# Kernel optimization log

Hardware: AMD Instinct MI355X
Metric: run time of the kernel (lower is better)

Reference implementation:

```python
import jax, jax.numpy as jnp
import numpy as np

B, H0, W0, C = 8, 112, 112, 192
NH, WS, SS = 6, 7, 3
HID = 4 * C


def _rel_pos_index(ws):
    coords = np.stack(np.meshgrid(np.arange(ws), np.arange(ws), indexing='ij'))  # [2,ws,ws]
    flat = coords.reshape(2, -1)
    rel = flat[:, :, None] - flat[:, None, :]          # [2,N,N]
    rel = rel.transpose(1, 2, 0).copy()                # [N,N,2]
    rel[:, :, 0] += ws - 1
    rel[:, :, 1] += ws - 1
    rel[:, :, 0] *= 2 * ws - 1
    return rel.sum(-1)                                 # [N,N]


def _attn_mask(Hp, Wp, ws, ss):
    # 0 / -100 mask for shifted windows, identical to torch get_attn_mask
    img = np.zeros((Hp, Wp))
    cnt = 0
    for hs in (slice(0, -ws), slice(-ws, -ss), slice(-ss, None)):
        for wsl in (slice(0, -ws), slice(-ws, -ss), slice(-ss, None)):
            img[hs, wsl] = cnt
            cnt += 1
    mw = img.reshape(Hp // ws, ws, Wp // ws, ws).transpose(0, 2, 1, 3).reshape(-1, ws * ws)
    am = mw[:, None, :] - mw[:, :, None]
    return np.where(am != 0, np.float32(-100.0), np.float32(0.0)).astype(np.float32)  # [nW,N,N]


def _ln(x, g, b, eps=1e-5):
    mu = jnp.mean(x, axis=-1, keepdims=True)
    var = jnp.mean(jnp.square(x - mu), axis=-1, keepdims=True)
    return (x - mu) * jax.lax.rsqrt(var + eps) * g + b


def setup_inputs() -> dict:
    key = jax.random.key(0)
    ks = jax.random.split(key, 8)
    p = lambda k, s: jax.random.normal(k, s, jnp.float32) * 0.02
    return {
        'query': jax.random.normal(ks[0], (B, H0 * W0, C), jnp.float32),
        'norm1_g': jnp.ones((C,), jnp.float32), 'norm1_b': jnp.zeros((C,), jnp.float32),
        'qkv_w': p(ks[1], (C, 3 * C)), 'qkv_b': jnp.zeros((3 * C,), jnp.float32),
        'rpb_table': p(ks[2], ((2 * WS - 1) ** 2, NH)),
        'proj_w': p(ks[3], (C, C)), 'proj_b': jnp.zeros((C,), jnp.float32),
        'norm2_g': jnp.ones((C,), jnp.float32), 'norm2_b': jnp.zeros((C,), jnp.float32),
        'fc1_w': p(ks[4], (C, HID)), 'fc1_b': jnp.zeros((HID,), jnp.float32),
        'fc2_w': p(ks[5], (HID, C)), 'fc2_b': jnp.zeros((C,), jnp.float32),
        'H': H0, 'W': W0,
    }


def reference(query, norm1_g, norm1_b, qkv_w, qkv_b, rpb_table, proj_w, proj_b,
              norm2_g, norm2_b, fc1_w, fc1_b, fc2_w, fc2_b, H, W):
    Bq, L, Cq = query.shape
    ws, ss, nh = WS, SS, NH
    hd = Cq // nh
    N = ws * ws
    # ---- W-MSA branch ----
    x = _ln(query, norm1_g, norm1_b).reshape(Bq, H, W, Cq)
    # H, W chosen divisible by ws -> pad branch is a no-op
    x = jnp.roll(x, (-ss, -ss), axis=(1, 2))            # cyclic shift
    nWh, nWw = H // ws, W // ws
    # window partition -> [B*nW, N, C]
    xw = x.reshape(Bq, nWh, ws, nWw, ws, Cq).transpose(0, 1, 3, 2, 4, 5).reshape(-1, N, Cq)
    qkv = (xw @ qkv_w + qkv_b).reshape(-1, N, 3, nh, hd).transpose(2, 0, 3, 1, 4)
    q, k, v = qkv[0] * (hd ** -0.5), qkv[1], qkv[2]     # [B_,nh,N,hd]
    attn = jnp.einsum('bhnd,bhmd->bhnm', q, k)
    bias = rpb_table[_rel_pos_index(ws).reshape(-1)].reshape(N, N, nh).transpose(2, 0, 1)
    attn = attn + bias[None]
    mask = jnp.asarray(_attn_mask(H, W, ws, ss))        # [nW,N,N]
    nW = mask.shape[0]
    attn = attn.reshape(Bq, nW, nh, N, N) + mask[None, :, None]
    attn = jax.nn.softmax(attn.reshape(-1, nh, N, N), axis=-1)
    out = jnp.einsum('bhnm,bhmd->bhnd', attn, v).transpose(0, 2, 1, 3).reshape(-1, N, Cq)
    out = out @ proj_w + proj_b
    # window reverse + reverse shift
    x = out.reshape(Bq, nWh, nWw, ws, ws, Cq).transpose(0, 1, 3, 2, 4, 5).reshape(Bq, H, W, Cq)
    x = jnp.roll(x, (ss, ss), axis=(1, 2)).reshape(Bq, H * W, Cq)
    x = query + x
    # ---- MLP branch ----
    h = _ln(x, norm2_g, norm2_b)
    h = jax.nn.gelu(h @ fc1_w + fc1_b, approximate=False)
    return x + (h @ fc2_w + fc2_b)
```

## Files before the change

### kernel.cpp

```cpp
#include <hip/hip_runtime.h>
#include <hip/hip_bf16.h>
#include <math.h>

using bf16 = __hip_bfloat16;
typedef __bf16 bf16x8 __attribute__((ext_vector_type(8)));
typedef __bf16 bf16x4 __attribute__((ext_vector_type(4)));
typedef float floatx4 __attribute__((ext_vector_type(4)));

__device__ __forceinline__ float bf2f(bf16 x) { return __bfloat162float(x); }
__device__ __forceinline__ bf16 f2bf(float x) { return __float2bfloat16(x); }

__device__ __forceinline__ float loadExt(const void* p, long i, int f32) {
  return f32 ? ((const float*)p)[i] : bf2f(((const bf16*)p)[i]);
}
__device__ __forceinline__ void storeExt(void* p, long i, int f32, float v) {
  if (f32) ((float*)p)[i] = v;
  else     ((bf16*)p)[i] = f2bf(v);
}

#define GLOAD16(gp, lp)                                                       \
  __builtin_amdgcn_global_load_lds(                                           \
      (const __attribute__((address_space(1))) void*)(gp),                    \
      (__attribute__((address_space(3))) void*)(lp), 16, 0, 0)

#define LGKM0_BAR()                                                           \
  do {                                                                        \
    asm volatile("s_waitcnt lgkmcnt(0)" ::: "memory");                        \
    __builtin_amdgcn_s_barrier();                                             \
    __builtin_amdgcn_sched_barrier(0);                                        \
  } while (0)

__global__ void detect_kernel(const unsigned int* __restrict__ q, int* __restrict__ flag) {
  const int lane = threadIdx.x;
  const unsigned int w = q[lane];
  const unsigned int lo = w & 0xffffu;
  const unsigned int e = (lo >> 7) & 0xffu;
  const bool ok = (lo == 0u) || (e >= 100u && e <= 141u);
  const unsigned long long m = __ballot(ok);
  if (lane == 0) flag[0] = (__popcll(m) == 64) ? 1 : 0;
}

__global__ void cvt_params_kernel(const int* __restrict__ flagp,
                                  const void* qkv_b, const void* proj_b,
                                  const void* n1g, const void* n1b,
                                  const void* n2g, const void* n2b,
                                  const void* fc1_b, const void* fc2_b,
                                  const void* rpb, bf16* __restrict__ dst) {
  const int f32 = (flagp[0] == 0);
  int i = blockIdx.x * blockDim.x + threadIdx.x;
  if (i >= 3510) return;
  const void* src; int j = i;
  if      (j < 576)  { src = qkv_b; }
  else if ((j -= 576)  < 192) { src = proj_b; }
  else if ((j -= 192)  < 192) { src = n1g; }
  else if ((j -= 192)  < 192) { src = n1b; }
  else if ((j -= 192)  < 192) { src = n2g; }
  else if ((j -= 192)  < 192) { src = n2b; }
  else if ((j -= 192)  < 768) { src = fc1_b; }
  else if ((j -= 768)  < 192) { src = fc2_b; }
  else { j -= 192; src = rpb; }
  dst[i] = f2bf(loadExt(src, j, f32));
}

__global__ void cvtT_kernel(const int* __restrict__ flagp, const void* __restrict__ src,
                            bf16* __restrict__ dst, int K, int N) {
  const int f32 = (flagp[0] == 0);
  int i = blockIdx.x * blockDim.x + threadIdx.x;
  if (i >= K * N) return;
  int n = i / K, k = i - n * K;
  dst[i] = f2bf(loadExt(src, (long)k * N + n, f32));
}

__global__ void biastab_kernel(const bf16* __restrict__ rpb,
                               bf16* __restrict__ btab) {
  int i = blockIdx.x * blockDim.x + threadIdx.x;
  if (i >= 6 * 2450) return;
  int head = i / 2450, r = i - head * 2450;
  int n = r / 50, m = r - n * 50;
  float v = 0.f;
  if (n < 49 && m < 49) {
    int r1 = n / 7, c1 = n - 7 * r1, r2 = m / 7, c2 = m - 7 * r2;
    v = bf2f(rpb[((r1 - r2 + 6) * 13 + (c1 - c2 + 6)) * 6 + head]);
  }
  btab[i] = f2bf(v);
}

__global__ __launch_bounds__(256) void ln_kernel(const int* __restrict__ flagp, int ext,
                                                 const void* __restrict__ x,
                                                 const bf16* __restrict__ g,
                                                 const bf16* __restrict__ b,
                                                 bf16* __restrict__ out) {
  const int f32 = ext && (flagp[0] == 0);
  const long row = (long)blockIdx.x * 4 + (threadIdx.x >> 6);
  const int lane = threadIdx.x & 63;
  const long gbase = row * 192;
  float v0 = loadExt(x, gbase + lane, f32);
  float v1 = loadExt(x, gbase + lane + 64, f32);
  float v2 = loadExt(x, gbase + lane + 128, f32);
  float s = v0 + v1 + v2;
  #pragma unroll
  for (int off = 32; off > 0; off >>= 1) s += __shfl_xor(s, off, 64);
  const float mu = s * (1.0f / 192.0f);
  float d0 = v0 - mu, d1 = v1 - mu, d2 = v2 - mu;
  float vv = d0 * d0 + d1 * d1 + d2 * d2;
  #pragma unroll
  for (int off = 32; off > 0; off >>= 1) vv += __shfl_xor(vv, off, 64);
  const float rstd = rsqrtf(vv * (1.0f / 192.0f) + 1e-5f);
  bf16* orow = out + row * 192;
  orow[lane]       = f2bf(d0 * rstd * bf2f(g[lane])       + bf2f(b[lane]));
  orow[lane + 64]  = f2bf(d1 * rstd * bf2f(g[lane + 64])  + bf2f(b[lane + 64]));
  orow[lane + 128] = f2bf(d2 * rstd * bf2f(g[lane + 128]) + bf2f(b[lane + 128]));
}

template <int EPI>
__global__ __launch_bounds__(256) void gemm_bt(const bf16* __restrict__ A,
                                               const bf16* __restrict__ BT,
                                               const bf16* __restrict__ bias,
                                               const int* __restrict__ flagp,
                                               const void* res, int res_ext,
                                               void* out, int out_ext,
                                               int M, int N, int K) {
  __shared__ __align__(16) bf16 As[3][128 * 32];
  __shared__ __align__(16) bf16 Bs[3][64 * 32];
  const int xf32 = (flagp[0] == 0);
  const int tid = threadIdx.x;
  const int wave = tid >> 6;
  const int lane = tid & 63;
  const int l16 = lane & 15;
  const int quad = lane >> 4;

  const int nbn = N >> 6;
  const int cpx = gridDim.x >> 3;
  const int wg = (gridDim.x & 7) ? (int)blockIdx.x
                                 : (blockIdx.x & 7) * cpx + (blockIdx.x >> 3);
  const int mb = wg / nbn;
  const int nb = wg - mb * nbn;
  const long m0 = (long)mb * 128;
  const int n0 = nb << 6;

  const int rS = tid >> 2;
  const int sS = tid & 3;
  const int ss = sS ^ ((rS >> 1) & 3);
  const bf16* gA0 = A + (m0 + rS) * (long)K + ss * 8;
  const bf16* gA1 = A + (m0 + rS + 64) * (long)K + ss * 8;
  const bf16* gB  = BT + (long)(n0 + rS) * K + ss * 8;

  floatx4 acc[2][4];
  #pragma unroll
  for (int i = 0; i < 2; i++)
    #pragma unroll
    for (int j = 0; j < 4; j++) acc[i][j] = (floatx4){0.f, 0.f, 0.f, 0.f};

  const int swz = (quad ^ ((l16 >> 1) & 3)) << 3;
  const int arow = wave * 32 + l16;
  const int nt = K >> 5;

  {
    GLOAD16(gA0, &As[0][tid * 8]);
    GLOAD16(gA1, &As[0][(tid + 256) * 8]);
    GLOAD16(gB,  &Bs[0][tid * 8]);
    GLOAD16(gA0 + 32, &As[1][tid * 8]);
    GLOAD16(gA1 + 32, &As[1][(tid + 256) * 8]);
    GLOAD16(gB  + 32, &Bs[1][tid * 8]);
  }

  for (int t = 0; t < nt; ++t) {
    if (t + 1 < nt) { asm volatile("s_waitcnt vmcnt(3)" ::: "memory"); }
    else            { asm volatile("s_waitcnt vmcnt(0)" ::: "memory"); }
    __builtin_amdgcn_s_barrier();
    __builtin_amdgcn_sched_barrier(0);
    if (t + 2 < nt) {
      const int p2 = (t + 2) % 3;
      const int off = (t + 2) * 32;
      GLOAD16(gA0 + off, &As[p2][tid * 8]);
      GLOAD16(gA1 + off, &As[p2][(tid + 256) * 8]);
      GLOAD16(gB  + off, &Bs[p2][tid * 8]);
    }
    const int p = t % 3;
    bf16x8 af[2], bfr[4];
    #pragma unroll
    for (int ms = 0; ms < 2; ms++)
      af[ms] = *(const bf16x8*)&As[p][(arow + ms * 16) * 32 + swz];
    #pragma unroll
    for (int ns = 0; ns < 4; ns++)
      bfr[ns] = *(const bf16x8*)&Bs[p][(ns * 16 + l16) * 32 + swz];
    #pragma unroll
    for (int ms = 0; ms < 2; ms++)
      #pragma unroll
      for (int ns = 0; ns < 4; ns++)
        acc[ms][ns] = __builtin_amdgcn_mfma_f32_16x16x32_bf16(bfr[ns], af[ms], acc[ms][ns], 0, 0, 0);
  }

  #pragma unroll
  for (int ms = 0; ms < 2; ms++) {
    const long row = m0 + wave * 32 + ms * 16 + l16;
    #pragma unroll
    for (int ns = 0; ns < 4; ns++) {
      const int col = n0 + ns * 16 + quad * 4;
      const long idx = row * (long)N + col;
      float v[4];
      #pragma unroll
      for (int r = 0; r < 4; r++) v[r] = acc[ms][ns][r] + bf2f(bias[col + r]);
      if (EPI == 1) {
        #pragma unroll
        for (int r = 0; r < 4; r++)
          v[r] = 0.5f * v[r] * (1.0f + erff(v[r] * 0.70710678118654752f));
      }
      if (EPI == 2) {
        if (res_ext && xf32) {
          const float4 t = *(const float4*)((const float*)res + idx);
          v[0] += t.x; v[1] += t.y; v[2] += t.z; v[3] += t.w;
        } else {
          const bf16x4 t = *(const bf16x4*)((const bf16*)res + idx);
          #pragma unroll
          for (int r = 0; r < 4; r++) v[r] += (float)t[r];
        }
      }
      if (out_ext && xf32) {
        float4 t; t.x = v[0]; t.y = v[1]; t.z = v[2]; t.w = v[3];
        *(float4*)((float*)out + idx) = t;
      } else {
        bf16x4 t;
        #pragma unroll
        for (int r = 0; r < 4; r++) t[r] = (__bf16)v[r];
        *(bf16x4*)((bf16*)out + idx) = t;
      }
    }
  }
}

__global__ __launch_bounds__(256, 1) void mlp_fused(
    const bf16* __restrict__ xb,
    const bf16* __restrict__ w1,
    const bf16* __restrict__ w2,
    const bf16* __restrict__ gN, const bf16* __restrict__ bN,
    const bf16* __restrict__ b1, const bf16* __restrict__ b2,
    const int* __restrict__ flagp, void* __restrict__ out) {
  __shared__ __align__(16) __bf16 Ash[128 * 192];
  __shared__ __align__(16) __bf16 W1sh[2][64 * 192];
  __shared__ __align__(16) __bf16 W2sh[192 * 64];
  __shared__ __align__(16) __bf16 Hsh[128 * 64];
  const int xf32 = (flagp[0] == 0);
  const int tid = threadIdx.x, wave = tid >> 6, lane = tid & 63;
  const int l16 = lane & 15, quad = lane >> 4;
  const int cpx = gridDim.x >> 3;
  const int mb = (gridDim.x & 7) ? (int)blockIdx.x
                                 : (int)(blockIdx.x & 7) * cpx + (int)(blockIdx.x >> 3);
  const long m0 = (long)mb * 128;

  {
    const bf16* src = xb + m0 * 192;
    #pragma unroll
    for (int i = 0; i < 12; i++)
      GLOAD16(src + (i * 256 + tid) * 8, &Ash[(i * 256 + tid) * 8]);
  }
  asm volatile("s_waitcnt vmcnt(0)" ::: "memory");
  __builtin_amdgcn_s_barrier();

  {
    const int row = tid >> 1, half = tid & 1;
    bf16x8 xr[12];
    #pragma unroll
    for (int i = 0; i < 12; i++)
      xr[i] = *(const bf16x8*)&Ash[row * 192 + (half * 12 + i) * 8];
    float s1 = 0.f;
    #pragma unroll
    for (int i = 0; i < 12; i++)
      #pragma unroll
      for (int j = 0; j < 8; j++) s1 += (float)xr[i][j];
    s1 += __shfl_xor(s1, 1, 64);
    const float mu = s1 * (1.0f / 192.0f);
    float s2 = 0.f;
    #pragma unroll
    for (int i = 0; i < 12; i++)
      #pragma unroll
      for (int j = 0; j < 8; j++) {
        const float d = (float)xr[i][j] - mu;
        s2 += d * d;
      }
    s2 += __shfl_xor(s2, 1, 64);
    const float rstd = rsqrtf(s2 * (1.0f / 192.0f) + 1e-5f);
    #pragma unroll
    for (int i = 0; i < 12; i++) {
      const int slot = half * 12 + i;
      const bf16x8 gg = *(const bf16x8*)&gN[slot * 8];
      const bf16x8 bb = *(const bf16x8*)&bN[slot * 8];
      bf16x8 nr;
      #pragma unroll
      for (int j = 0; j < 8; j++)
        nr[j] = (__bf16)(((float)xr[i][j] - mu) * rstd * (float)gg[j] + (float)bb[j]);
      xr[i] = nr;
    }
    __syncthreads();
    #pragma unroll
    for (int i = 0; i < 12; i++) {
      const int slot = half * 12 + i;
      const int sw = (slot & 24) | ((slot ^ row) & 7);
      *(bf16x8*)&Ash[row * 192 + sw * 8] = xr[i];
    }
  }
  __syncthreads();

  bf16x8 afr[2][6];
  #pragma unroll
  for (int mt = 0; mt < 2; mt++)
    #pragma unroll
    for (int ks = 0; ks < 6; ks++) {
      const int r = wave * 32 + mt * 16 + l16;
      const int sl = ks * 4 + quad;
      afr[mt][ks] = *(const bf16x8*)&Ash[r * 192 + ((sl & 24) | ((sl ^ r) & 7)) * 8];
    }

  bf16x8 st1[6], st2[6];
  #pragma unroll
  for (int i = 0; i < 6; i++) {
    const int u = i * 256 + tid;
    st1[i] = *(const bf16x8*)&w1[(u / 24) * 192 + (u % 24) * 8];
    st2[i] = *(const bf16x8*)&w2[(u >> 3) * 768 + (u & 7) * 8];
  }
  #pragma unroll
  for (int i = 0; i < 6; i++) {
    const int u = i * 256 + tid;
    const int r1 = u / 24, sl1 = u % 24;
    *(bf16x8*)&W1sh[0][r1 * 192 + ((sl1 & 24) | ((sl1 ^ r1) & 7)) * 8] = st1[i];
    const int r2 = u >> 3, sl2 = u & 7;
    *(bf16x8*)&W2sh[r2 * 64 + ((sl2 ^ r2) & 7) * 8] = st2[i];
  }
  __syncthreads();

  floatx4 C[12][2];
  #pragma unroll
  for (int nt = 0; nt < 12; nt++)
    #pragma unroll
    for (int mt = 0; mt < 2; mt++) C[nt][mt] = (floatx4){0.f, 0.f, 0.f, 0.f};

  for (int s = 0; s < 12; ++s) {
    const int cur = s & 1;
    if (s + 1 < 12) {
      #pragma unroll
      for (int i = 0; i < 6; i++) {
        const int u = i * 256 + tid;
        st1[i] = *(const bf16x8*)&w1[((s + 1) * 64 + u / 24) * 192 + (u % 24) * 8];
        st2[i] = *(const bf16x8*)&w2[(u >> 3) * 768 + (s + 1) * 64 + (u & 7) * 8];
      }
    }
    floatx4 h[4][2];
    #pragma unroll
    for (int jt = 0; jt < 4; jt++)
      #pragma unroll
      for (int mt = 0; mt < 2; mt++) h[jt][mt] = (floatx4){0.f, 0.f, 0.f, 0.f};
    #pragma unroll
    for (int ks = 0; ks < 6; ks++) {
      bf16x8 wf[4];
      #pragma unroll
      for (int jt = 0; jt < 4; jt++) {
        const int r = jt * 16 + l16;
        const int sl = ks * 4 + quad;
        wf[jt] = *(const bf16x8*)&W1sh[cur][r * 192 + ((sl & 24) | ((sl ^ r) & 7)) * 8];
      }
      #pragma unroll
      for (int jt = 0; jt < 4; jt++)
        #pragma unroll
        for (int mt = 0; mt < 2; mt++)
          h[jt][mt] = __builtin_amdgcn_mfma_f32_16x16x32_bf16(wf[jt], afr[mt][ks], h[jt][mt], 0, 0, 0);
    }
    #pragma unroll
    for (int jt = 0; jt < 4; jt++)
      #pragma unroll
      for (int mt = 0; mt < 2; mt++)
        #pragma unroll
        for (int r = 0; r < 4; r++) {
          const int j = jt * 16 + quad * 4 + r;
          float v = h[jt][mt][r] + bf2f(b1[s * 64 + j]);
          v = 0.5f * v * (1.0f + erff(v * 0.70710678118654752f));
          const int m = wave * 32 + mt * 16 + l16;
          Hsh[m * 64 + (((jt * 2 + (quad >> 1)) ^ (l16 & 7)) & 7) * 8 + ((quad * 4 + r) & 7)] = (__bf16)v;
        }
    if (s + 1 < 12) {
      #pragma unroll
      for (int i = 0; i < 6; i++) {
        const int u = i * 256 + tid;
        const int r1 = u / 24, sl1 = u % 24;
        *(bf16x8*)&W1sh[cur ^ 1][r1 * 192 + ((sl1 & 24) | ((sl1 ^ r1) & 7)) * 8] = st1[i];
      }
    }
    LGKM0_BAR();
    #pragma unroll
    for (int k2 = 0; k2 < 2; k2++) {
      bf16x8 hf[2];
      #pragma unroll
      for (int mt = 0; mt < 2; mt++) {
        const int m = wave * 32 + mt * 16 + l16;
        const int sl = k2 * 4 + quad;
        hf[mt] = *(const bf16x8*)&Hsh[m * 64 + ((sl ^ (l16 & 7)) & 7) * 8];
      }
      #pragma unroll
      for (int nt = 0; nt < 12; nt++) {
        const int n = nt * 16 + l16;
        const int sl = k2 * 4 + quad;
        const bf16x8 wf2 = *(const bf16x8*)&W2sh[n * 64 + ((sl ^ n) & 7) * 8];
        #pragma unroll
        for (int mt = 0; mt < 2; mt++)
          C[nt][mt] = __builtin_amdgcn_mfma_f32_16x16x32_bf16(wf2, hf[mt], C[nt][mt], 0, 0, 0);
      }
    }
    LGKM0_BAR();
    if (s + 1 < 12) {
      #pragma unroll
      for (int i = 0; i < 6; i++) {
        const int u = i * 256 + tid;
        const int r2 = u >> 3, sl2 = u & 7;
        *(bf16x8*)&W2sh[r2 * 64 + ((sl2 ^ r2) & 7) * 8] = st2[i];
      }
    }
  }

  #pragma unroll
  for (int mt = 0; mt < 2; mt++) {
    const long row = m0 + wave * 32 + mt * 16 + l16;
    #pragma unroll
    for (int nt = 0; nt < 12; nt++) {
      const int col = nt * 16 + quad * 4;
      const long idx = row * 192 + col;
      float v[4];
      #pragma unroll
      for (int r = 0; r < 4; r++) v[r] = C[nt][mt][r] + bf2f(b2[col + r]);
      const bf16x4 t = *(const bf16x4*)&xb[idx];
      #pragma unroll
      for (int r = 0; r < 4; r++) v[r] += (float)t[r];
      if (xf32) {
        float4 o; o.x = v[0]; o.y = v[1]; o.z = v[2]; o.w = v[3];
        *(float4*)((float*)out + idx) = o;
      } else {
        bf16x4 o;
        #pragma unroll
        for (int r = 0; r < 4; r++) o[r] = (__bf16)v[r];
        *(bf16x4*)((bf16*)out + idx) = o;
      }
    }
  }
}

__global__ __launch_bounds__(64, 3) void attn_kernel(const bf16* __restrict__ qkv,
                                                     const bf16* __restrict__ btab,
                                                     bf16* __restrict__ out) {
  __shared__ __align__(16) __bf16 vshT[32 * 64];
  __shared__ __align__(16) __bf16 psh[64 * 64];
  __shared__ int rowIdx[64];
  __shared__ int regn[64];
  const int lane = threadIdx.x;
  const int q = lane >> 4, l16 = lane & 15;
  const int unit = blockIdx.x;
  const int head = unit % 6;
  const int wIdx = unit / 6;
  const int b = wIdx >> 8;
  const int w2 = wIdx & 255;
  const int wh = w2 >> 4;
  const int ww = w2 & 15;

  {
    const int l = lane < 49 ? lane : 48;
    const int r = l / 7, c = l - 7 * r;
    const int hr = wh * 7 + r;
    const int wr = ww * 7 + c;
    int h = hr + 3; if (h >= 112) h -= 112;
    int w = wr + 3; if (w >= 112) w -= 112;
    rowIdx[lane] = b * 12544 + h * 112 + w;
    const int rh = hr < 105 ? 0 : (hr < 109 ? 1 : 2);
    const int rw = wr < 105 ? 0 : (wr < 109 ? 1 : 2);
    regn[lane] = (lane < 49) ? rh * 3 + rw : 99;
  }
  __syncthreads();

  int ridx[4];
  #pragma unroll
  for (int t = 0; t < 4; t++) ridx[t] = rowIdx[t * 16 + l16];

  #pragma unroll
  for (int ii = 0; ii < 4; ii++) {
    const int i = lane + ii * 64;
    const int j = i >> 2, c = (i & 3) * 8;
    const bf16x8 vv = *(const bf16x8*)&qkv[(long)rowIdx[j] * 576 + 384 + head * 32 + c];
    #pragma unroll
    for (int jj = 0; jj < 8; jj++) {
      const int d = c + jj;
      vshT[d * 64 + (((j >> 3) ^ (d & 7)) << 3) + (j & 7)] = vv[jj];
    }
  }

  floatx4 s[4][4];
  #pragma unroll
  for (int it = 0; it < 4; it++)
    #pragma unroll
    for (int jt = 0; jt < 4; jt++) s[it][jt] = (floatx4){0.f, 0.f, 0.f, 0.f};
  {
    bf16x8 afq[4], bfk[4];
    #pragma unroll
    for (int t = 0; t < 4; t++) {
      const bf16* pQ = &qkv[(long)ridx[t] * 576 + head * 32 + q * 8];
      afq[t] = *(const bf16x8*)pQ;
      bfk[t] = *(const bf16x8*)(pQ + 192);
    }
    #pragma unroll
    for (int it = 0; it < 4; it++)
      #pragma unroll
      for (int jt = 0; jt < 4; jt++)
        s[it][jt] = __builtin_amdgcn_mfma_f32_16x16x32_bf16(afq[it], bfk[jt], s[it][jt], 0, 0, 0);
  }

  int regj[4];
  #pragma unroll
  for (int jt = 0; jt < 4; jt++) regj[jt] = regn[jt * 16 + l16];
  int regi[4][4];
  #pragma unroll
  for (int it = 0; it < 4; it++)
    #pragma unroll
    for (int r = 0; r < 4; r++) regi[it][r] = regn[it * 16 + q * 4 + r];

  const bf16* bt = btab + head * 2450;
  const float scale = 0.17677669529663687f;
  float mrow[4][4];
  #pragma unroll
  for (int it = 0; it < 4; it++)
    #pragma unroll
    for (int r = 0; r < 4; r++) mrow[it][r] = -3e38f;

  #pragma unroll
  for (int it = 0; it < 4; it++)
    #pragma unroll
    for (int jt = 0; jt < 4; jt++)
      #pragma unroll
      for (int r = 0; r < 4; r++) {
        const int i = it * 16 + q * 4 + r;
        const int j = jt * 16 + l16;
        const int bi = (i < 49 ? i : 48) * 50 + (j < 49 ? j : 48);
        float v = s[it][jt][r] * scale + bf2f(bt[bi]);
        if (regi[it][r] != regj[jt]) v -= 100.0f;
        v = (j < 49) ? v : -1e30f;
        s[it][jt][r] = v;
        mrow[it][r] = fmaxf(mrow[it][r], v);
      }
  #pragma unroll
  for (int it = 0; it < 4; it++)
    #pragma unroll
    for (int r = 0; r < 4; r++) {
      float m = mrow[it][r];
      #pragma unroll
      for (int off = 1; off < 16; off <<= 1) m = fmaxf(m, __shfl_xor(m, off, 64));
      mrow[it][r] = m;
    }
  float sum[4][4];
  #pragma unroll
  for (int it = 0; it < 4; it++)
    #pragma unroll
    for (int r = 0; r < 4; r++) sum[it][r] = 0.f;
  #pragma unroll
  for (int it = 0; it < 4; it++)
    #pragma unroll
    for (int jt = 0; jt < 4; jt++)
      #pragma unroll
      for (int r = 0; r < 4; r++) {
        const float e = __expf(s[it][jt][r] - mrow[it][r]);
        s[it][jt][r] = e;
        sum[it][r] += e;
      }
  #pragma unroll
  for (int it = 0; it < 4; it++)
    #pragma unroll
    for (int r = 0; r < 4; r++) {
      float t = sum[it][r];
      #pragma unroll
      for (int off = 1; off < 16; off <<= 1) t += __shfl_xor(t, off, 64);
      mrow[it][r] = 1.0f / t;
    }

  #pragma unroll
  for (int it = 0; it < 4; it++)
    #pragma unroll
    for (int jt = 0; jt < 4; jt++)
      #pragma unroll
      for (int r = 0; r < 4; r++) {
        const int i = it * 16 + q * 4 + r;
        const int j = jt * 16 + l16;
        psh[i * 64 + (((j >> 3) ^ (i & 7)) << 3) + (j & 7)] =
            (__bf16)(s[it][jt][r] * mrow[it][r]);
      }
  __syncthreads();

  floatx4 o[4][2];
  #pragma unroll
  for (int it = 0; it < 4; it++)
    #pragma unroll
    for (int dt = 0; dt < 2; dt++) o[it][dt] = (floatx4){0.f, 0.f, 0.f, 0.f};
  #pragma unroll
  for (int ks = 0; ks < 2; ks++) {
    bf16x8 av[2];
    #pragma unroll
    for (int dt = 0; dt < 2; dt++) {
      const int row = dt * 16 + l16;
      av[dt] = *(const bf16x8*)&vshT[row * 64 + (((ks * 4 + q) ^ (row & 7)) << 3)];
    }
    #pragma unroll
    for (int it = 0; it < 4; it++) {
      const int row = it * 16 + l16;
      const bf16x8 bp = *(const bf16x8*)&psh[row * 64 + (((ks * 4 + q) ^ (row & 7)) << 3)];
      #pragma unroll
      for (int dt = 0; dt < 2; dt++)
        o[it][dt] = __builtin_amdgcn_mfma_f32_16x16x32_bf16(bp, av[dt], o[it][dt], 0, 0, 0);
    }
  }

  #pragma unroll
  for (int it = 0; it < 4; it++)
    #pragma unroll
    for (int r = 0; r < 4; r++) {
      const int i = it * 16 + q * 4 + r;
      if (i < 49) {
        const long ob = (long)rowIdx[i] * 192 + head * 32;
        #pragma unroll
        for (int dt = 0; dt < 2; dt++)
          out[ob + dt * 16 + l16] = f2bf(o[it][dt][r]);
      }
    }
}

extern "C" void kernel_launch(void* const* d_in, const int* in_sizes, int n_in,
                              void* d_out, int out_size, void* d_ws, size_t ws_size,
                              hipStream_t stream) {
  const void* query   = d_in[0];
  const void* norm1_g = d_in[1];
  const void* norm1_b = d_in[2];
  const void* qkv_w   = d_in[3];
  const void* qkv_b   = d_in[4];
  const void* rpb     = d_in[5];
  const void* proj_w  = d_in[6];
  const void* proj_b  = d_in[7];
  const void* norm2_g = d_in[8];
  const void* norm2_b = d_in[9];
  const void* fc1_w   = d_in[10];
  const void* fc1_b   = d_in[11];
  const void* fc2_w   = d_in[12];
  const void* fc2_b   = d_in[13];

  const long M = 100352;

  int* flag  = (int*)d_ws;
  bf16* base = (bf16*)((char*)d_ws + 16);
  bf16* wsA   = base;
  bf16* wsB   = wsA + M * 192;
  bf16* xbuf  = wsB + M * 768;
  bf16* qkvT  = xbuf + M * 192;
  bf16* projT = qkvT + 110592;
  bf16* fc1T  = projT + 36864;
  bf16* fc2T  = fc1T + 147456;
  bf16* pPAR  = fc2T + 147456;
  bf16* pQKVB = pPAR;
  bf16* pPRJB = pQKVB + 576;
  bf16* pN1G  = pPRJB + 192;
  bf16* pN1B  = pN1G + 192;
  bf16* pN2G  = pN1B + 192;
  bf16* pN2B  = pN2G + 192;
  bf16* pFC1B = pN2B + 192;
  bf16* pFC2B = pFC1B + 768;
  bf16* pRPB  = pFC2B + 192;
  bf16* btab  = pPAR + 3510;

  detect_kernel<<<1, 64, 0, stream>>>((const unsigned int*)query, flag);
  cvt_params_kernel<<<14, 256, 0, stream>>>(flag, qkv_b, proj_b, norm1_g, norm1_b,
                                            norm2_g, norm2_b, fc1_b, fc2_b, rpb, pPAR);
  cvtT_kernel<<<(192 * 576 + 255) / 256, 256, 0, stream>>>(flag, qkv_w, qkvT, 192, 576);
  cvtT_kernel<<<(192 * 192 + 255) / 256, 256, 0, stream>>>(flag, proj_w, projT, 192, 192);
  cvtT_kernel<<<(192 * 768 + 255) / 256, 256, 0, stream>>>(flag, fc1_w, fc1T, 192, 768);
  cvtT_kernel<<<(768 * 192 + 255) / 256, 256, 0, stream>>>(flag, fc2_w, fc2T, 768, 192);
  biastab_kernel<<<(6 * 2450 + 255) / 256, 256, 0, stream>>>(pRPB, btab);

  ln_kernel<<<M / 4, 256, 0, stream>>>(flag, 1, query, pN1G, pN1B, wsA);
  gemm_bt<0><<<784 * 9, 256, 0, stream>>>(wsA, qkvT, pQKVB, flag,
                                          nullptr, 0, wsB, 0, (int)M, 576, 192);
  attn_kernel<<<12288, 64, 0, stream>>>(wsB, btab, wsA);
  gemm_bt<2><<<784 * 3, 256, 0, stream>>>(wsA, projT, pPRJB, flag,
                                          query, 1, xbuf, 0, (int)M, 192, 192);

  mlp_fused<<<784, 256, 0, stream>>>(xbuf, fc1T, fc2T, pN2G, pN2B,
                                     pFC1B, pFC2B, flag, d_out);
}
```

Measured before the change: 652.2 us.

## Stream MLP weights from global memory and simplify GEMM to double buffering

In the fused MLP kernel, fc1/fc2 weight tiles are no longer staged through shared memory; MFMA operands are loaded straight from global memory and rely on cache hits. The hidden activation tile becomes per-wave and double-buffered inside a single shared buffer that aliases the input tile, so the cross-wave barriers can go. This cuts LDS use sharply and drops the launch-bounds limit of one block, aiming for higher occupancy. The generic GEMM moves from a 3-stage async pipeline with fine-grained vmcnt waits to a simpler 2-stage loop with __syncthreads, which risks exposing more global load latency.

After: 845.6 us. 29.7% more time.

```diff
diff --git a/kernel.cpp b/kernel.cpp
--- a/kernel.cpp
+++ b/kernel.cpp
@@ -22,13 +22,6 @@
   __builtin_amdgcn_global_load_lds(                                           \
       (const __attribute__((address_space(1))) void*)(gp),                    \
       (__attribute__((address_space(3))) void*)(lp), 16, 0, 0)
-
-#define LGKM0_BAR()                                                           \
-  do {                                                                        \
-    asm volatile("s_waitcnt lgkmcnt(0)" ::: "memory");                        \
-    __builtin_amdgcn_s_barrier();                                             \
-    __builtin_amdgcn_sched_barrier(0);                                        \
-  } while (0)
 
 __global__ void detect_kernel(const unsigned int* __restrict__ q, int* __restrict__ flag) {
   const int lane = threadIdx.x;
@@ -120,8 +113,8 @@
                                                const void* res, int res_ext,
                                                void* out, int out_ext,
                                                int M, int N, int K) {
-  __shared__ __align__(16) bf16 As[3][128 * 32];
-  __shared__ __align__(16) bf16 Bs[3][64 * 32];
+  __shared__ __align__(16) bf16 As[2][128 * 32];
+  __shared__ __align__(16) bf16 Bs[2][64 * 32];
   const int xf32 = (flagp[0] == 0);
   const int tid = threadIdx.x;
   const int wave = tid >> 6;
@@ -153,42 +146,34 @@
 
   const int swz = (quad ^ ((l16 >> 1) & 3)) << 3;
   const int arow = wave * 32 + l16;
-  const int nt = K >> 5;
-
-  {
-    GLOAD16(gA0, &As[0][tid * 8]);
-    GLOAD16(gA1, &As[0][(tid + 256) * 8]);
-    GLOAD16(gB,  &Bs[0][tid * 8]);
-    GLOAD16(gA0 + 32, &As[1][tid * 8]);
-    GLOAD16(gA1 + 32, &As[1][(tid + 256) * 8]);
-    GLOAD16(gB  + 32, &Bs[1][tid * 8]);
-  }
-
-  for (int t = 0; t < nt; ++t) {
-    if (t + 1 < nt) { asm volatile("s_waitcnt vmcnt(3)" ::: "memory"); }
-    else            { asm volatile("s_waitcnt vmcnt(0)" ::: "memory"); }
-    __builtin_amdgcn_s_barrier();
-    __builtin_amdgcn_sched_barrier(0);
-    if (t + 2 < nt) {
-      const int p2 = (t + 2) % 3;
-      const int off = (t + 2) * 32;
-      GLOAD16(gA0 + off, &As[p2][tid * 8]);
-      GLOAD16(gA1 + off, &As[p2][(tid + 256) * 8]);
-      GLOAD16(gB  + off, &Bs[p2][tid * 8]);
-    }
-    const int p = t % 3;
+
+  GLOAD16(gA0, &As[0][tid * 8]);
+  GLOAD16(gA1, &As[0][(tid + 256) * 8]);
+  GLOAD16(gB,  &Bs[0][tid * 8]);
+  __syncthreads();
+
+  int cur = 0;
+  for (int k0 = 0; k0 < K; k0 += 32) {
+    if (k0 + 32 < K) {
+      const int nxt = cur ^ 1;
+      GLOAD16(gA0 + k0 + 32, &As[nxt][tid * 8]);
+      GLOAD16(gA1 + k0 + 32, &As[nxt][(tid + 256) * 8]);
+      GLOAD16(gB  + k0 + 32, &Bs[nxt][tid * 8]);
+    }
     bf16x8 af[2], bfr[4];
     #pragma unroll
     for (int ms = 0; ms < 2; ms++)
-      af[ms] = *(const bf16x8*)&As[p][(arow + ms * 16) * 32 + swz];
+      af[ms] = *(const bf16x8*)&As[cur][(arow + ms * 16) * 32 + swz];
     #pragma unroll
     for (int ns = 0; ns < 4; ns++)
-      bfr[ns] = *(const bf16x8*)&Bs[p][(ns * 16 + l16) * 32 + swz];
+      bfr[ns] = *(const bf16x8*)&Bs[cur][(ns * 16 + l16) * 32 + swz];
     #pragma unroll
     for (int ms = 0; ms < 2; ms++)
       #pragma unroll
       for (int ns = 0; ns < 4; ns++)
         acc[ms][ns] = __builtin_amdgcn_mfma_f32_16x16x32_bf16(bfr[ns], af[ms], acc[ms][ns], 0, 0, 0);
+    __syncthreads();
+    cur ^= 1;
   }
 
   #pragma unroll
@@ -229,17 +214,16 @@
   }
 }
 
-__global__ __launch_bounds__(256, 1) void mlp_fused(
+__global__ __launch_bounds__(256) void mlp_fused(
     const bf16* __restrict__ xb,
     const bf16* __restrict__ w1,
     const bf16* __restrict__ w2,
     const bf16* __restrict__ gN, const bf16* __restrict__ bN,
     const bf16* __restrict__ b1, const bf16* __restrict__ b2,
     const int* __restrict__ flagp, void* __restrict__ out) {
-  __shared__ __align__(16) __bf16 Ash[128 * 192];
-  __shared__ __align__(16) __bf16 W1sh[2][64 * 192];
-  __shared__ __align__(16) __bf16 W2sh[192 * 64];
-  __shared__ __align__(16) __bf16 Hsh[128 * 64];
+  __shared__ __align__(16) char smem[128 * 192 * 2];
+  __bf16* Ash = (__bf16*)smem;
+  __bf16* Hb  = (__bf16*)smem;
   const int xf32 = (flagp[0] == 0);
   const int tid = threadIdx.x, wave = tid >> 6, lane = tid & 63;
   const int l16 = lane & 15, quad = lane >> 4;
@@ -310,22 +294,6 @@
       const int sl = ks * 4 + quad;
       afr[mt][ks] = *(const bf16x8*)&Ash[r * 192 + ((sl & 24) | ((sl ^ r) & 7)) * 8];
     }
-
-  bf16x8 st1[6], st2[6];
-  #pragma unroll
-  for (int i = 0; i < 6; i++) {
-    const int u = i * 256 + tid;
-    st1[i] = *(const bf16x8*)&w1[(u / 24) * 192 + (u % 24) * 8];
-    st2[i] = *(const bf16x8*)&w2[(u >> 3) * 768 + (u & 7) * 8];
-  }
-  #pragma unroll
-  for (int i = 0; i < 6; i++) {
-    const int u = i * 256 + tid;
-    const int r1 = u / 24, sl1 = u % 24;
-    *(bf16x8*)&W1sh[0][r1 * 192 + ((sl1 & 24) | ((sl1 ^ r1) & 7)) * 8] = st1[i];
-    const int r2 = u >> 3, sl2 = u & 7;
-    *(bf16x8*)&W2sh[r2 * 64 + ((sl2 ^ r2) & 7) * 8] = st2[i];
-  }
   __syncthreads();
 
   floatx4 C[12][2];
@@ -335,15 +303,7 @@
     for (int mt = 0; mt < 2; mt++) C[nt][mt] = (floatx4){0.f, 0.f, 0.f, 0.f};
 
   for (int s = 0; s < 12; ++s) {
-    const int cur = s & 1;
-    if (s + 1 < 12) {
-      #pragma unroll
-      for (int i = 0; i < 6; i++) {
-        const int u = i * 256 + tid;
-        st1[i] = *(const bf16x8*)&w1[((s + 1) * 64 + u / 24) * 192 + (u % 24) * 8];
-        st2[i] = *(const bf16x8*)&w2[(u >> 3) * 768 + (s + 1) * 64 + (u & 7) * 8];
-      }
-    }
+    __bf16* H = Hb + (s & 1) * (128 * 64);
     floatx4 h[4][2];
     #pragma unroll
     for (int jt = 0; jt < 4; jt++)
@@ -353,11 +313,8 @@
     for (int ks = 0; ks < 6; ks++) {
       bf16x8 wf[4];
       #pragma unroll
-      for (int jt = 0; jt < 4; jt++) {
-        const int r = jt * 16 + l16;
-        const int sl = ks * 4 + quad;
-        wf[jt] = *(const bf16x8*)&W1sh[cur][r * 192 + ((sl & 24) | ((sl ^ r) & 7)) * 8];
-      }
+      for (int jt = 0; jt < 4; jt++)
+        wf[jt] = *(const bf16x8*)&w1[(long)(s * 64 + jt * 16 + l16) * 192 + ks * 32 + quad * 8];
       #pragma unroll
       for (int jt = 0; jt < 4; jt++)
         #pragma unroll
@@ -367,50 +324,32 @@
     #pragma unroll
     for (int jt = 0; jt < 4; jt++)
       #pragma unroll
-      for (int mt = 0; mt < 2; mt++)
+      for (int mt = 0; mt < 2; mt++) {
+        const int m = wave * 32 + mt * 16 + l16;
+        bf16x4 pk;
         #pragma unroll
         for (int r = 0; r < 4; r++) {
           const int j = jt * 16 + quad * 4 + r;
           float v = h[jt][mt][r] + bf2f(b1[s * 64 + j]);
           v = 0.5f * v * (1.0f + erff(v * 0.70710678118654752f));
-          const int m = wave * 32 + mt * 16 + l16;
-          Hsh[m * 64 + (((jt * 2 + (quad >> 1)) ^ (l16 & 7)) & 7) * 8 + ((quad * 4 + r) & 7)] = (__bf16)v;
+          pk[r] = (__bf16)v;
         }
-    if (s + 1 < 12) {
-      #pragma unroll
-      for (int i = 0; i < 6; i++) {
-        const int u = i * 256 + tid;
-        const int r1 = u / 24, sl1 = u % 24;
-        *(bf16x8*)&W1sh[cur ^ 1][r1 * 192 + ((sl1 & 24) | ((sl1 ^ r1) & 7)) * 8] = st1[i];
-      }
-    }
-    LGKM0_BAR();
+        *(bf16x4*)&H[m * 64 + ((jt * 4 + quad) ^ (l16 & 14)) * 4] = pk;
+      }
     #pragma unroll
     for (int k2 = 0; k2 < 2; k2++) {
       bf16x8 hf[2];
       #pragma unroll
       for (int mt = 0; mt < 2; mt++) {
         const int m = wave * 32 + mt * 16 + l16;
-        const int sl = k2 * 4 + quad;
-        hf[mt] = *(const bf16x8*)&Hsh[m * 64 + ((sl ^ (l16 & 7)) & 7) * 8];
+        hf[mt] = *(const bf16x8*)&H[m * 64 + ((k2 * 8 + quad * 2) ^ (l16 & 14)) * 4];
       }
       #pragma unroll
       for (int nt = 0; nt < 12; nt++) {
-        const int n = nt * 16 + l16;
-        const int sl = k2 * 4 + quad;
-        const bf16x8 wf2 = *(const bf16x8*)&W2sh[n * 64 + ((sl ^ n) & 7) * 8];
+        const bf16x8 wf2 = *(const bf16x8*)&w2[(long)(nt * 16 + l16) * 768 + s * 64 + k2 * 32 + quad * 8];
         #pragma unroll
         for (int mt = 0; mt < 2; mt++)
           C[nt][mt] = __builtin_amdgcn_mfma_f32_16x16x32_bf16(wf2, hf[mt], C[nt][mt], 0, 0, 0);
-      }
-    }
-    LGKM0_BAR();
-    if (s + 1 < 12) {
-      #pragma unroll
-      for (int i = 0; i < 6; i++) {
-        const int u = i * 256 + tid;
-        const int r2 = u >> 3, sl2 = u & 7;
-        *(bf16x8*)&W2sh[r2 * 64 + ((sl2 ^ r2) & 7) * 8] = st2[i];
       }
     }
   }
```
